# Optimization experiments

Measured on AMD Instinct MI355X. Metric: run time of the kernel, lower is better.

## Reference

```python
import jax, jax.numpy as jnp
import numpy as np

EMB = 1024
HEADS = 16
QKV = 64
INNER = 2816  # 256 * ceil(2*1024*4/3 / 256)


def rms_norm(x, w, eps=1e-6):
    xf = x.astype(jnp.float32)
    n = xf * jax.lax.rsqrt(jnp.mean(xf * xf, axis=-1, keepdims=True) + eps)
    return n.astype(x.dtype) * w


def setup_inputs() -> dict:
    key = jax.random.key(0)
    ks = jax.random.split(key, 12)
    s = 0.02
    return {
        "x": jax.random.normal(ks[0], (4, 2048, EMB), dtype=jnp.float32),
        "Wq": jax.random.normal(ks[1], (HEADS * QKV, EMB), dtype=jnp.float32) * s,
        "Wk": jax.random.normal(ks[2], (HEADS * QKV, EMB), dtype=jnp.float32) * s,
        "Wv": jax.random.normal(ks[3], (HEADS * QKV, EMB), dtype=jnp.float32) * s,
        "Wc": jax.random.normal(ks[4], (EMB, HEADS * QKV), dtype=jnp.float32) * s,
        "bc": jnp.zeros((EMB,), dtype=jnp.float32),
        "g1": jnp.ones((EMB,), dtype=jnp.float32),
        "g2": jnp.ones((EMB,), dtype=jnp.float32),
        "L1": jax.random.normal(ks[5], (INNER, EMB), dtype=jnp.float32) * s,
        "L2": jax.random.normal(ks[6], (INNER, EMB), dtype=jnp.float32) * s,
        "L3": jax.random.normal(ks[7], (EMB, INNER), dtype=jnp.float32) * s,
    }


def reference(x, Wq, Wk, Wv, Wc, bc, g1, g2, L1, L2, L3):
    B, N, D = x.shape
    # QKV projections (torch Linear: y = x @ W.T), split into heads: [B,H,N,dk]
    q = (x @ Wq.T).reshape(B, N, HEADS, QKV).transpose(0, 2, 1, 3)
    k = (x @ Wk.T).reshape(B, N, HEADS, QKV).transpose(0, 2, 1, 3)
    v = (x @ Wv.T).reshape(B, N, HEADS, QKV).transpose(0, 2, 1, 3)
    # attention: explicit score matrix [B,H,N,N]
    score = jnp.einsum("bhnd,bhmd->bhnm", q, k) / jnp.sqrt(jnp.float32(QKV))
    weights = jax.nn.softmax(score, axis=-1)
    out = jnp.einsum("bhnm,bhmd->bhnd", weights, v)
    out = out.transpose(0, 2, 1, 3).reshape(B, N, HEADS * QKV)
    mha = out @ Wc.T + bc
    h = rms_norm(x + mha, g1)
    # parallel gated MLP: silu(h@L1.T) * (h@L2.T) @ L3.T
    ff = (jax.nn.silu(h @ L1.T) * (h @ L2.T)) @ L3.T
    return rms_norm(h + ff, g2)
```

## Files before the change

kernel.cpp:

```cpp
#include <hip/hip_runtime.h>
#include <hip/hip_bf16.h>


#define EMB   1024
#define HEADS 16
#define DK    64
#define INNER 2816
#define BATCH 4
#define NTOK  2048
#define MROWS (BATCH * NTOK)

#define QSCALE 0.18033688011112042f

typedef short bf16x8 __attribute__((ext_vector_type(8)));
typedef short s16x4  __attribute__((ext_vector_type(4)));
typedef float f32x4  __attribute__((ext_vector_type(4)));

typedef const void __attribute__((address_space(1)))* gas_cvp;
typedef void       __attribute__((address_space(3)))* las_vp;

__device__ __forceinline__ short to_bf16(float f) {
  union { float f; unsigned u; } x; x.f = f;
  unsigned r = x.u + 0x7FFFu + ((x.u >> 16) & 1u);
  return (short)(r >> 16);
}

__device__ __forceinline__ unsigned cvt_pk_bf16(float a, float b) {
  unsigned r;
  asm("v_cvt_pk_bf16_f32 %0, %1, %2" : "=v"(r) : "v"(a), "v"(b));
  return r;
}

__device__ __forceinline__ void gld16(void* lds, const void* g) {
  __builtin_amdgcn_global_load_lds((gas_cvp)g, (las_vp)lds, 16, 0, 0);
}

__global__ __launch_bounds__(256, 4)
void cvtk(const float* __restrict__ s, short* __restrict__ d, int n4) {
  int i = blockIdx.x * 256 + threadIdx.x;
  if (i < n4) {
    float4 v = ((const float4*)s)[i];
    s16x4 o;
    o[0] = to_bf16(v.x); o[1] = to_bf16(v.y);
    o[2] = to_bf16(v.z); o[3] = to_bf16(v.w);
    ((s16x4*)d)[i] = o;
  }
}

__global__ __launch_bounds__(256, 4)
void cvt_inter(const float* __restrict__ L1, const float* __restrict__ L2,
               short* __restrict__ d) {
  int i = blockIdx.x * 256 + threadIdx.x;
  if (i >= INNER * 256) return;
  int row = i >> 8, c4 = i & 255;
  float4 v1 = ((const float4*)L1)[i];
  float4 v2 = ((const float4*)L2)[i];
  s16x4 o1, o2;
  o1[0]=to_bf16(v1.x); o1[1]=to_bf16(v1.y); o1[2]=to_bf16(v1.z); o1[3]=to_bf16(v1.w);
  o2[0]=to_bf16(v2.x); o2[1]=to_bf16(v2.y); o2[2]=to_bf16(v2.z); o2[3]=to_bf16(v2.w);
  ((s16x4*)d)[(size_t)(2 * row) * 256 + c4]     = o1;
  ((s16x4*)d)[(size_t)(2 * row + 1) * 256 + c4] = o2;
}

template<int MODE>
__global__ __launch_bounds__(256, 2)
void gemm_bt(const short* __restrict__ A, const short* __restrict__ Bw,
             int M, int N, int K,
             void* __restrict__ out0, void* __restrict__ out1,
             void* __restrict__ out2,
             const float* __restrict__ aux0, const float* __restrict__ aux1)
{
  __shared__ short At[128 * 64];
  __shared__ short Bt[128 * 64];
  const int t = threadIdx.x;
  const int lane = t & 63;
  const int l15 = lane & 15, lhi = lane >> 4;
  const int w  = t >> 6;
  const int wm = (w >> 1) << 6;
  const int wn = (w & 1) << 6;
  const int tilesN = N >> 7;
  const int m0 = (blockIdx.x / tilesN) << 7;
  const int n0 = (blockIdx.x % tilesN) << 7;

  const int r = t >> 3;
  const int p = t & 7;
  const int psrc = p ^ (r & 7);
  const short* Ag = A  + (size_t)(m0 + r) * K + psrc * 8;
  const short* Bg = Bw + (size_t)(n0 + r) * K + psrc * 8;

  f32x4 acc[4][4];
  const f32x4 fz = {0.f, 0.f, 0.f, 0.f};
#pragma unroll
  for (int i = 0; i < 4; i++)
#pragma unroll
    for (int j = 0; j < 4; j++) acc[i][j] = fz;

  int aoff[2][4], boff[2][4];
#pragma unroll
  for (int kk = 0; kk < 2; kk++)
#pragma unroll
    for (int mt = 0; mt < 4; mt++) {
      int ra = wm + mt * 16 + l15;
      aoff[kk][mt] = ra * 128 + ((kk * 64 + lhi * 16) ^ ((ra & 7) << 4));
      int rb = wn + mt * 16 + l15;
      boff[kk][mt] = rb * 128 + ((kk * 64 + lhi * 16) ^ ((rb & 7) << 4));
    }

  for (int k0 = 0; k0 < K; k0 += 64) {
#pragma unroll
    for (int i = 0; i < 4; i++) {
      gld16((char*)At + t * 16 + i * 4096, Ag + (size_t)i * 32 * K + k0);
      gld16((char*)Bt + t * 16 + i * 4096, Bg + (size_t)i * 32 * K + k0);
    }
    __syncthreads();
#pragma unroll
    for (int kk = 0; kk < 2; kk++) {
      bf16x8 a[4], b[4];
#pragma unroll
      for (int mt = 0; mt < 4; mt++)
        a[mt] = *(const bf16x8*)((const char*)At + aoff[kk][mt]);
#pragma unroll
      for (int nt = 0; nt < 4; nt++)
        b[nt] = *(const bf16x8*)((const char*)Bt + boff[kk][nt]);
#pragma unroll
      for (int mt = 0; mt < 4; mt++)
#pragma unroll
        for (int nt = 0; nt < 4; nt++)
          acc[mt][nt] = __builtin_amdgcn_mfma_f32_16x16x32_bf16(
              a[mt], b[nt], acc[mt][nt], 0, 0, 0);
    }
    __syncthreads();
  }

#pragma unroll
  for (int mt = 0; mt < 4; mt++) {
#pragma unroll
    for (int nt = 0; nt < 4; nt++) {
      const int mb = m0 + wm + mt * 16 + lhi * 4;
      const int n  = n0 + wn + nt * 16 + l15;
      if constexpr (MODE == 0) {
        const int which = n >> 10, c = n & 1023;
        if (which == 2) {
          const int hh = c >> 6, dd = c & 63;
          const int bb = mb >> 11, tok = mb & 2047;
          s16x4 pk;
#pragma unroll
          for (int j = 0; j < 4; j++) pk[j] = to_bf16(acc[mt][nt][j]);
          *(s16x4*)((short*)out2 +
                    (size_t)((bb * HEADS + hh) * DK + dd) * NTOK + tok) = pk;
        } else {
          short* dst = (which == 0) ? (short*)out0 : (short*)out1;
          const float scl = (which == 0) ? QSCALE : 1.0f;
#pragma unroll
          for (int j = 0; j < 4; j++)
            dst[(size_t)(mb + j) * 1024 + c] = to_bf16(acc[mt][nt][j] * scl);
        }
      } else if constexpr (MODE == 1) {
#pragma unroll
        for (int j = 0; j < 4; j++) {
          size_t idx = (size_t)(mb + j) * 1024 + n;
          ((float*)out0)[idx] = acc[mt][nt][j] + aux1[n] + aux0[idx];
        }
      } else if constexpr (MODE == 2) {
#pragma unroll
        for (int j = 0; j < 4; j++) {
          float v0 = acc[mt][nt][j];
          float v1 = __shfl_xor(v0, 1);
          if ((lane & 1) == 0) {
            float su = v0 / (1.f + __expf(-v0));
            ((short*)out0)[(size_t)(mb + j) * INNER + (n >> 1)] =
                to_bf16(su * v1);
          }
        }
      } else {
#pragma unroll
        for (int j = 0; j < 4; j++) {
          size_t idx = (size_t)(mb + j) * 1024 + n;
          ((float*)out0)[idx] = acc[mt][nt][j] + aux0[idx];
        }
      }
    }
  }
}

__global__ __launch_bounds__(256, 2)
void attn_k(const short* __restrict__ qb, const short* __restrict__ kb,
            const short* __restrict__ vtb, short* __restrict__ ob)
{
  __shared__ short Kt[64 * 64];
  __shared__ short Vt[64 * 64];
  __shared__ short Pt[64 * 64];
  const int t = threadIdx.x;
  const int lane = t & 63;
  const int l15 = lane & 15, lhi = lane >> 4;
  const int w = t >> 6;
  const int bh = blockIdx.x;
  const int b = bh >> 4, h = bh & 15;
  const int q0 = blockIdx.y << 6;
  const int qrow = q0 + w * 16 + l15;

  bf16x8 aq[2];
  {
    const short* qp = qb + (size_t)(b * NTOK + qrow) * EMB + h * DK + lhi * 8;
    aq[0] = *(const bf16x8*)qp;
    aq[1] = *(const bf16x8*)(qp + 32);
  }

  f32x4 acc_o[4];
  const f32x4 fz = {0.f, 0.f, 0.f, 0.f};
#pragma unroll
  for (int dt = 0; dt < 4; dt++) acc_o[dt] = fz;
  float m_run = -1e30f, l_run = 0.f;

  const int r = t >> 3, p = t & 7;
  const int psrc = p ^ (r & 7);
  const short* kg = kb  + (size_t)(b * NTOK + r) * EMB + h * DK + psrc * 8;
  const short* vg = vtb + (size_t)(bh * DK + r) * NTOK + psrc * 8;

  int kvoff[4][2];
#pragma unroll
  for (int x = 0; x < 4; x++)
#pragma unroll
    for (int kk = 0; kk < 2; kk++) {
      int row = x * 16 + l15;
      kvoff[x][kk] = row * 128 + ((kk * 64 + lhi * 16) ^ ((row & 7) << 4));
    }
  const int prow = w * 16 + l15;
  int pwoff[4], proff[2];
#pragma unroll
  for (int kvt = 0; kvt < 4; kvt++)
    pwoff[kvt] = prow * 128 + ((kvt * 32 + lhi * 8) ^ ((prow & 7) << 4));
#pragma unroll
  for (int kk = 0; kk < 2; kk++)
    proff[kk] = prow * 128 + ((kk * 64 + lhi * 16) ^ ((prow & 7) << 4));

  for (int kv0 = 0; kv0 < NTOK; kv0 += 64) {
    __syncthreads();
#pragma unroll
    for (int i = 0; i < 2; i++) {
      gld16((char*)Kt + t * 16 + i * 4096, kg + (size_t)(kv0 + i * 32) * EMB);
      gld16((char*)Vt + t * 16 + i * 4096, vg + (size_t)i * 32 * NTOK + kv0);
    }
    __syncthreads();

    f32x4 s[4];
#pragma unroll
    for (int kvt = 0; kvt < 4; kvt++) {
      s[kvt] = fz;
#pragma unroll
      for (int kk = 0; kk < 2; kk++) {
        bf16x8 ak = *(const bf16x8*)((const char*)Kt + kvoff[kvt][kk]);
        s[kvt] = __builtin_amdgcn_mfma_f32_16x16x32_bf16(ak, aq[kk], s[kvt], 0, 0, 0);
      }
    }
    float mx = fmaxf(fmaxf(fmaxf(s[0][0], s[0][1]), fmaxf(s[0][2], s[0][3])),
                     fmaxf(fmaxf(s[1][0], s[1][1]), fmaxf(s[1][2], s[1][3])));
    float mx2 = fmaxf(fmaxf(fmaxf(s[2][0], s[2][1]), fmaxf(s[2][2], s[2][3])),
                      fmaxf(fmaxf(s[3][0], s[3][1]), fmaxf(s[3][2], s[3][3])));
    mx = fmaxf(mx, mx2);
    mx = fmaxf(mx, __shfl_xor(mx, 16));
    mx = fmaxf(mx, __shfl_xor(mx, 32));
    const float mnew = fmaxf(m_run, mx);
    const float alpha = exp2f(m_run - mnew);
    m_run = mnew;
    float sum = 0.f;
#pragma unroll
    for (int kvt = 0; kvt < 4; kvt++)
#pragma unroll
      for (int j = 0; j < 4; j++) {
        float pe = exp2f(s[kvt][j] - mnew);
        s[kvt][j] = pe;
        sum += pe;
      }
    sum += __shfl_xor(sum, 16);
    sum += __shfl_xor(sum, 32);
    l_run = l_run * alpha + sum;
#pragma unroll
    for (int dt = 0; dt < 4; dt++)
#pragma unroll
      for (int j = 0; j < 4; j++) acc_o[dt][j] *= alpha;

#pragma unroll
    for (int kvt = 0; kvt < 4; kvt++) {
      uint2 uu;
      uu.x = cvt_pk_bf16(s[kvt][0], s[kvt][1]);
      uu.y = cvt_pk_bf16(s[kvt][2], s[kvt][3]);
      *(uint2*)((char*)Pt + pwoff[kvt]) = uu;
    }
    bf16x8 pb[2];
#pragma unroll
    for (int kk = 0; kk < 2; kk++)
      pb[kk] = *(const bf16x8*)((const char*)Pt + proff[kk]);
#pragma unroll
    for (int dt = 0; dt < 4; dt++)
#pragma unroll
      for (int kk = 0; kk < 2; kk++) {
        bf16x8 av = *(const bf16x8*)((const char*)Vt + kvoff[dt][kk]);
        acc_o[dt] = __builtin_amdgcn_mfma_f32_16x16x32_bf16(av, pb[kk], acc_o[dt], 0, 0, 0);
      }
  }

  const float inv = 1.f / l_run;
  short* op = ob + (size_t)(b * NTOK + qrow) * EMB + h * DK;
#pragma unroll
  for (int dt = 0; dt < 4; dt++) {
    s16x4 pk;
#pragma unroll
    for (int j = 0; j < 4; j++) pk[j] = to_bf16(acc_o[dt][j] * inv);
    *(s16x4*)(op + dt * 16 + lhi * 4) = pk;
  }
}

template<bool WB>
__global__ __launch_bounds__(256, 4)
void rmsnorm_k(const float* __restrict__ in, const float* __restrict__ gw,
               float* __restrict__ of, short* __restrict__ ob)
{
  const int row = blockIdx.x;
  const int t = threadIdx.x;
  const float4 v = ((const float4*)(in + (size_t)row * EMB))[t];
  float ss = v.x * v.x + v.y * v.y + v.z * v.z + v.w * v.w;
#pragma unroll
  for (int off = 1; off < 64; off <<= 1) ss += __shfl_xor(ss, off);
  __shared__ float red[4];
  if ((t & 63) == 0) red[t >> 6] = ss;
  __syncthreads();
  float tot = red[0] + red[1] + red[2] + red[3];
  const float rinv = rsqrtf(tot * (1.f / EMB) + 1e-6f);
  const float4 g4 = ((const float4*)gw)[t];
  float4 o;
  o.x = v.x * rinv * g4.x; o.y = v.y * rinv * g4.y;
  o.z = v.z * rinv * g4.z; o.w = v.w * rinv * g4.w;
  ((float4*)(of + (size_t)row * EMB))[t] = o;
  if (WB) {
    s16x4 pk;
    pk[0] = to_bf16(o.x); pk[1] = to_bf16(o.y);
    pk[2] = to_bf16(o.z); pk[3] = to_bf16(o.w);
    ((s16x4*)(ob + (size_t)row * EMB))[t] = pk;
  }
}

extern "C" void kernel_launch(void* const* d_in, const int* in_sizes, int n_in,
                              void* d_out, int out_size, void* d_ws, size_t ws_size,
                              hipStream_t stream)
{
  const float* x  = (const float*)d_in[0];
  const float* Wq = (const float*)d_in[1];
  const float* Wk = (const float*)d_in[2];
  const float* Wv = (const float*)d_in[3];
  const float* Wc = (const float*)d_in[4];
  const float* bc = (const float*)d_in[5];
  const float* g1 = (const float*)d_in[6];
  const float* g2 = (const float*)d_in[7];
  const float* L1 = (const float*)d_in[8];
  const float* L2 = (const float*)d_in[9];
  const float* L3 = (const float*)d_in[10];
  float* out = (float*)d_out;

  char* ws = (char*)d_ws;
  size_t o = 0;
  auto take = [&](size_t bytes) -> char* {
    char* pp = ws + o;
    o += (bytes + 255) & ~(size_t)255;
    return pp;
  };
  short* xb   = (short*)take((size_t)MROWS * EMB * 2);
  short* wqkv = (short*)take((size_t)3072 * 1024 * 2);
  short* wcb  = (short*)take((size_t)1024 * 1024 * 2);
  short* l12  = (short*)take((size_t)5632 * 1024 * 2);
  short* l3b  = (short*)take((size_t)1024 * 2816 * 2);
  short* q    = (short*)take((size_t)MROWS * EMB * 2);
  short* k    = (short*)take((size_t)MROWS * EMB * 2);
  short* v    = (short*)take((size_t)MROWS * EMB * 2);
  short* attn = (short*)take((size_t)MROWS * EMB * 2);
  float* t1   = (float*)take((size_t)MROWS * EMB * 4);
  float* h32  = (float*)take((size_t)MROWS * EMB * 4);
  short* hb   = (short*)take((size_t)MROWS * EMB * 2);
  short* gated = q;
  float* t2    = t1;

  cvtk<<<MROWS * EMB / 4 / 256, 256, 0, stream>>>(x, xb, MROWS * EMB / 4);
  cvtk<<<1024 * 1024 / 4 / 256, 256, 0, stream>>>(Wq, wqkv, 1024 * 1024 / 4);
  cvtk<<<1024 * 1024 / 4 / 256, 256, 0, stream>>>(Wk, wqkv + 1024 * 1024, 1024 * 1024 / 4);
  cvtk<<<1024 * 1024 / 4 / 256, 256, 0, stream>>>(Wv, wqkv + 2 * 1024 * 1024, 1024 * 1024 / 4);
  cvtk<<<1024 * 1024 / 4 / 256, 256, 0, stream>>>(Wc, wcb, 1024 * 1024 / 4);
  cvt_inter<<<INNER, 256, 0, stream>>>(L1, L2, l12);
  cvtk<<<1024 * 2816 / 4 / 256, 256, 0, stream>>>(L3, l3b, 1024 * 2816 / 4);

  gemm_bt<0><<<64 * 24, 256, 0, stream>>>(xb, wqkv, MROWS, 3072, 1024,
                                          q, k, v, nullptr, nullptr);
  attn_k<<<dim3(64, 32), 256, 0, stream>>>(q, k, v, attn);
  gemm_bt<1><<<64 * 8, 256, 0, stream>>>(attn, wcb, MROWS, 1024, 1024,
                                         t1, nullptr, nullptr, x, bc);
  rmsnorm_k<true><<<MROWS, 256, 0, stream>>>(t1, g1, h32, hb);
  gemm_bt<2><<<64 * 44, 256, 0, stream>>>(hb, l12, MROWS, 5632, 1024,
                                          gated, nullptr, nullptr, nullptr, nullptr);
  gemm_bt<3><<<64 * 8, 256, 0, stream>>>(gated, l3b, MROWS, 1024, 2816,
                                         t2, nullptr, nullptr, h32, nullptr);
  rmsnorm_k<false><<<MROWS, 256, 0, stream>>>(t2, g2, out, nullptr);
}
```

Measured before the change: 459.3 us.

## Double-buffer K/V tiles, process 128 query rows per block, lazy softmax rescale

The attention kernel now stages the next K/V tile into a second LDS buffer while computing on the current one, so global loads overlap with MFMA work. Each wave handles two 16-row query sets, which reuses every loaded K/V fragment twice and halves the grid. Softmax skips the rescale unless the running max grows by more than a threshold, and the row sum is reduced across lanes only once at the end. It also sets wave priority around the MFMA blocks and pads the P buffer instead of swizzling it. The costs are more registers and LDS per block and fewer blocks in the grid.

```diff
diff --git a/kernel.cpp b/kernel.cpp
--- a/kernel.cpp
+++ b/kernel.cpp
@@ -183,34 +183,38 @@
   }
 }
 
-__global__ __launch_bounds__(256, 2)
+__global__ __launch_bounds__(256, 3)
 void attn_k(const short* __restrict__ qb, const short* __restrict__ kb,
             const short* __restrict__ vtb, short* __restrict__ ob)
 {
-  __shared__ short Kt[64 * 64];
-  __shared__ short Vt[64 * 64];
-  __shared__ short Pt[64 * 64];
+  __shared__ short Kt[2][64 * 64];
+  __shared__ short Vt[2][64 * 64];
+  __shared__ short Pt[128 * 68];
   const int t = threadIdx.x;
   const int lane = t & 63;
   const int l15 = lane & 15, lhi = lane >> 4;
   const int w = t >> 6;
   const int bh = blockIdx.x;
   const int b = bh >> 4, h = bh & 15;
-  const int q0 = blockIdx.y << 6;
-  const int qrow = q0 + w * 16 + l15;
-
-  bf16x8 aq[2];
-  {
-    const short* qp = qb + (size_t)(b * NTOK + qrow) * EMB + h * DK + lhi * 8;
-    aq[0] = *(const bf16x8*)qp;
-    aq[1] = *(const bf16x8*)(qp + 32);
-  }
-
-  f32x4 acc_o[4];
+  const int q0 = blockIdx.y << 7;
+
+  bf16x8 aq[2][2];
+#pragma unroll
+  for (int s = 0; s < 2; s++) {
+    const short* qp = qb + (size_t)(b * NTOK + q0 + w * 32 + s * 16 + l15) * EMB
+                         + h * DK + lhi * 8;
+    aq[s][0] = *(const bf16x8*)qp;
+    aq[s][1] = *(const bf16x8*)(qp + 32);
+  }
+
+  f32x4 acc[2][4];
   const f32x4 fz = {0.f, 0.f, 0.f, 0.f};
 #pragma unroll
-  for (int dt = 0; dt < 4; dt++) acc_o[dt] = fz;
-  float m_run = -1e30f, l_run = 0.f;
+  for (int s = 0; s < 2; s++)
+#pragma unroll
+    for (int dt = 0; dt < 4; dt++) acc[s][dt] = fz;
+  float m_run[2] = {-1e30f, -1e30f};
+  float l_run[2] = {0.f, 0.f};
 
   const int r = t >> 3, p = t & 7;
   const int psrc = p ^ (r & 7);
@@ -225,89 +229,141 @@
       int row = x * 16 + l15;
       kvoff[x][kk] = row * 128 + ((kk * 64 + lhi * 16) ^ ((row & 7) << 4));
     }
-  const int prow = w * 16 + l15;
-  int pwoff[4], proff[2];
-#pragma unroll
-  for (int kvt = 0; kvt < 4; kvt++)
-    pwoff[kvt] = prow * 128 + ((kvt * 32 + lhi * 8) ^ ((prow & 7) << 4));
-#pragma unroll
-  for (int kk = 0; kk < 2; kk++)
-    proff[kk] = prow * 128 + ((kk * 64 + lhi * 16) ^ ((prow & 7) << 4));
-
-  for (int kv0 = 0; kv0 < NTOK; kv0 += 64) {
-    __syncthreads();
-#pragma unroll
-    for (int i = 0; i < 2; i++) {
-      gld16((char*)Kt + t * 16 + i * 4096, kg + (size_t)(kv0 + i * 32) * EMB);
-      gld16((char*)Vt + t * 16 + i * 4096, vg + (size_t)i * 32 * NTOK + kv0);
-    }
-    __syncthreads();
-
-    f32x4 s[4];
+  int pw[2][4], pr[2][2];
+#pragma unroll
+  for (int s = 0; s < 2; s++) {
+    const int prow = w * 32 + s * 16 + l15;
+#pragma unroll
+    for (int kvt = 0; kvt < 4; kvt++) pw[s][kvt] = prow * 136 + kvt * 32 + lhi * 8;
+#pragma unroll
+    for (int kk = 0; kk < 2; kk++)   pr[s][kk]  = prow * 136 + kk * 64 + lhi * 16;
+  }
+
+  auto stage = [&](short* Kd, short* Vd, int kv0) {
+    const short* ks = kg + (size_t)kv0 * EMB;
+    const short* vs = vg + kv0;
+    gld16(Kd + t * 8,        ks);
+    gld16(Kd + t * 8 + 2048, ks + (size_t)32 * EMB);
+    gld16(Vd + t * 8,        vs);
+    gld16(Vd + t * 8 + 2048, vs + (size_t)32 * NTOK);
+  };
+
+  auto do_set = [&](f32x4 (&sv)[4], float& mr, float& lr, f32x4 (&ac)[4],
+                    const int (&pwo)[4]) {
+    float pm = sv[0][0];
+#pragma unroll
+    for (int kvt = 0; kvt < 4; kvt++)
+#pragma unroll
+      for (int j = 0; j < 4; j++) pm = fmaxf(pm, sv[kvt][j]);
+    if (__any(pm > mr + 8.0f)) {
+      pm = fmaxf(pm, __shfl_xor(pm, 16));
+      pm = fmaxf(pm, __shfl_xor(pm, 32));
+      const float mnew = fmaxf(mr, pm);
+      const float al = exp2f(mr - mnew);
+      lr *= al;
+#pragma unroll
+      for (int dt = 0; dt < 4; dt++)
+#pragma unroll
+        for (int j = 0; j < 4; j++) ac[dt][j] *= al;
+      mr = mnew;
+    }
+    float ls = 0.f;
+#pragma unroll
+    for (int kvt = 0; kvt < 4; kvt++)
+#pragma unroll
+      for (int j = 0; j < 4; j++) {
+        float pe = exp2f(sv[kvt][j] - mr);
+        sv[kvt][j] = pe;
+        ls += pe;
+      }
+    lr += ls;
 #pragma unroll
     for (int kvt = 0; kvt < 4; kvt++) {
-      s[kvt] = fz;
-#pragma unroll
-      for (int kk = 0; kk < 2; kk++) {
-        bf16x8 ak = *(const bf16x8*)((const char*)Kt + kvoff[kvt][kk]);
-        s[kvt] = __builtin_amdgcn_mfma_f32_16x16x32_bf16(ak, aq[kk], s[kvt], 0, 0, 0);
-      }
-    }
-    float mx = fmaxf(fmaxf(fmaxf(s[0][0], s[0][1]), fmaxf(s[0][2], s[0][3])),
-                     fmaxf(fmaxf(s[1][0], s[1][1]), fmaxf(s[1][2], s[1][3])));
-    float mx2 = fmaxf(fmaxf(fmaxf(s[2][0], s[2][1]), fmaxf(s[2][2], s[2][3])),
-                      fmaxf(fmaxf(s[3][0], s[3][1]), fmaxf(s[3][2], s[3][3])));
-    mx = fmaxf(mx, mx2);
-    mx = fmaxf(mx, __shfl_xor(mx, 16));
-    mx = fmaxf(mx, __shfl_xor(mx, 32));
-    const float mnew = fmaxf(m_run, mx);
-    const float alpha = exp2f(m_run - mnew);
-    m_run = mnew;
-    float sum = 0.f;
-#pragma unroll
-    for (int kvt = 0; kvt < 4; kvt++)
-#pragma unroll
-      for (int j = 0; j < 4; j++) {
-        float pe = exp2f(s[kvt][j] - mnew);
-        s[kvt][j] = pe;
-        sum += pe;
-      }
-    sum += __shfl_xor(sum, 16);
-    sum += __shfl_xor(sum, 32);
-    l_run = l_run * alpha + sum;
+      uint2 u;
+      u.x = cvt_pk_bf16(sv[kvt][0], sv[kvt][1]);
+      u.y = cvt_pk_bf16(sv[kvt][2], sv[kvt][3]);
+      *(uint2*)((char*)Pt + pwo[kvt]) = u;
+    }
+  };
+
+  auto compute = [&](const short* Kb_, const short* Vb_) {
+    const char* Kb = (const char*)Kb_;
+    const char* Vb = (const char*)Vb_;
+    bf16x8 kf[4][2];
+#pragma unroll
+    for (int x = 0; x < 4; x++)
+#pragma unroll
+      for (int kk = 0; kk < 2; kk++)
+        kf[x][kk] = *(const bf16x8*)(Kb + kvoff[x][kk]);
+    f32x4 s0[4], s1[4];
+    __builtin_amdgcn_s_setprio(1);
+#pragma unroll
+    for (int kvt = 0; kvt < 4; kvt++) {
+      s0[kvt] = __builtin_amdgcn_mfma_f32_16x16x32_bf16(kf[kvt][0], aq[0][0], fz, 0, 0, 0);
+      s0[kvt] = __builtin_amdgcn_mfma_f32_16x16x32_bf16(kf[kvt][1], aq[0][1], s0[kvt], 0, 0, 0);
+      s1[kvt] = __builtin_amdgcn_mfma_f32_16x16x32_bf16(kf[kvt][0], aq[1][0], fz, 0, 0, 0);
+      s1[kvt] = __builtin_amdgcn_mfma_f32_16x16x32_bf16(kf[kvt][1], aq[1][1], s1[kvt], 0, 0, 0);
+    }
+    __builtin_amdgcn_s_setprio(0);
+    do_set(s0, m_run[0], l_run[0], acc[0], pw[0]);
+    do_set(s1, m_run[1], l_run[1], acc[1], pw[1]);
+    bf16x8 vf[4][2];
 #pragma unroll
     for (int dt = 0; dt < 4; dt++)
 #pragma unroll
-      for (int j = 0; j < 4; j++) acc_o[dt][j] *= alpha;
-
-#pragma unroll
-    for (int kvt = 0; kvt < 4; kvt++) {
-      uint2 uu;
-      uu.x = cvt_pk_bf16(s[kvt][0], s[kvt][1]);
-      uu.y = cvt_pk_bf16(s[kvt][2], s[kvt][3]);
-      *(uint2*)((char*)Pt + pwoff[kvt]) = uu;
-    }
-    bf16x8 pb[2];
-#pragma unroll
-    for (int kk = 0; kk < 2; kk++)
-      pb[kk] = *(const bf16x8*)((const char*)Pt + proff[kk]);
-#pragma unroll
-    for (int dt = 0; dt < 4; dt++)
-#pragma unroll
-      for (int kk = 0; kk < 2; kk++) {
-        bf16x8 av = *(const bf16x8*)((const char*)Vt + kvoff[dt][kk]);
-        acc_o[dt] = __builtin_amdgcn_mfma_f32_16x16x32_bf16(av, pb[kk], acc_o[dt], 0, 0, 0);
-      }
-  }
-
-  const float inv = 1.f / l_run;
-  short* op = ob + (size_t)(b * NTOK + qrow) * EMB + h * DK;
-#pragma unroll
-  for (int dt = 0; dt < 4; dt++) {
-    s16x4 pk;
-#pragma unroll
-    for (int j = 0; j < 4; j++) pk[j] = to_bf16(acc_o[dt][j] * inv);
-    *(s16x4*)(op + dt * 16 + lhi * 4) = pk;
+      for (int kk = 0; kk < 2; kk++)
+        vf[dt][kk] = *(const bf16x8*)(Vb + kvoff[dt][kk]);
+    bf16x8 pb0[2], pb1[2];
+#pragma unroll
+    for (int kk = 0; kk < 2; kk++) {
+      pb0[kk] = *(const bf16x8*)((const char*)Pt + pr[0][kk]);
+      pb1[kk] = *(const bf16x8*)((const char*)Pt + pr[1][kk]);
+    }
+    __builtin_amdgcn_s_setprio(1);
+#pragma unroll
+    for (int dt = 0; dt < 4; dt++) {
+#pragma unroll
+      for (int kk = 0; kk < 2; kk++)
+        acc[0][dt] = __builtin_amdgcn_mfma_f32_16x16x32_bf16(vf[dt][kk], pb0[kk], acc[0][dt], 0, 0, 0);
+#pragma unroll
+      for (int kk = 0; kk < 2; kk++)
+        acc[1][dt] = __builtin_amdgcn_mfma_f32_16x16x32_bf16(vf[dt][kk], pb1[kk], acc[1][dt], 0, 0, 0);
+    }
+    __builtin_amdgcn_s_setprio(0);
+  };
+
+  stage(Kt[0], Vt[0], 0);
+  for (int it = 0; it < 32; it += 2) {
+    stage(Kt[1], Vt[1], (it + 1) * 64);
+    asm volatile("s_waitcnt vmcnt(4)" ::: "memory");
+    __builtin_amdgcn_s_barrier();
+    compute(Kt[0], Vt[0]);
+    __builtin_amdgcn_s_barrier();
+    if (it + 2 < 32) {
+      stage(Kt[0], Vt[0], (it + 2) * 64);
+      asm volatile("s_waitcnt vmcnt(4)" ::: "memory");
+    } else {
+      asm volatile("s_waitcnt vmcnt(0)" ::: "memory");
+    }
+    __builtin_amdgcn_s_barrier();
+    compute(Kt[1], Vt[1]);
+    __builtin_amdgcn_s_barrier();
+  }
+
+#pragma unroll
+  for (int s = 0; s < 2; s++) {
+    float lt = l_run[s];
+    lt += __shfl_xor(lt, 16);
+    lt += __shfl_xor(lt, 32);
+    const float inv = 1.f / lt;
+    short* op = ob + (size_t)(b * NTOK + q0 + w * 32 + s * 16 + l15) * EMB + h * DK;
+#pragma unroll
+    for (int dt = 0; dt < 4; dt++) {
+      s16x4 pk;
+#pragma unroll
+      for (int j = 0; j < 4; j++) pk[j] = to_bf16(acc[s][dt][j] * inv);
+      *(s16x4*)(op + dt * 16 + lhi * 4) = pk;
+    }
   }
 }
 
@@ -389,7 +445,7 @@
 
   gemm_bt<0><<<64 * 24, 256, 0, stream>>>(xb, wqkv, MROWS, 3072, 1024,
                                           q, k, v, nullptr, nullptr);
-  attn_k<<<dim3(64, 32), 256, 0, stream>>>(q, k, v, attn);
+  attn_k<<<dim3(64, 16), 256, 0, stream>>>(q, k, v, attn);
   gemm_bt<1><<<64 * 8, 256, 0, stream>>>(attn, wcb, MROWS, 1024, 1024,
                                          t1, nullptr, nullptr, x, bc);
   rmsnorm_k<true><<<MROWS, 256, 0, stream>>>(t1, g1, h32, hb);
```

New measurement: 442.3 us. 1.04x faster.
